# Optimization experiments

Hardware: AMD Instinct MI355X
Metric: run time of the kernel (lower is better)

Reference implementation:

```python
import jax, jax.numpy as jnp
import numpy as np

B, LQ, LK, D, H, DFF = 2, 2048, 2048, 512, 8, 2048


def _xavier(key, shape):
    fan_in, fan_out = shape[0], shape[1]
    lim = float(np.sqrt(6.0 / (fan_in + fan_out)))
    return jax.random.uniform(key, shape, jnp.float32, -lim, lim)


def setup_inputs() -> dict:
    key = jax.random.key(0)
    ks = jax.random.split(key, 8)
    return {
        "inputs": jax.random.normal(ks[0], (B, LQ, D), jnp.float32),
        "encoder_x": jax.random.normal(ks[1], (B, LK, D), jnp.float32),
        "Wq": _xavier(ks[2], (D, D)),
        "Wk": _xavier(ks[3], (D, D)),
        "Wv": _xavier(ks[4], (D, D)),
        "ln1_g": jnp.ones((D,), jnp.float32),
        "ln1_b": jnp.zeros((D,), jnp.float32),
        "W1": jax.random.normal(ks[5], (D, DFF), jnp.float32) * 0.02,
        "b1": jnp.zeros((DFF,), jnp.float32),
        "W2": jax.random.normal(ks[6], (DFF, D), jnp.float32) * 0.02,
        "b2": jnp.zeros((D,), jnp.float32),
        "ln2_g": jnp.ones((D,), jnp.float32),
        "ln2_b": jnp.zeros((D,), jnp.float32),
        "n_heads": H,
    }


def _layer_norm(x, g, b, eps=1e-5):
    mu = jnp.mean(x, axis=-1, keepdims=True)
    var = jnp.var(x, axis=-1, keepdims=True)
    return (x - mu) * jax.lax.rsqrt(var + eps) * g + b


def reference(inputs, encoder_x, Wq, Wk, Wv, ln1_g, ln1_b, W1, b1, W2, b2, ln2_g, ln2_b, n_heads):
    b, lq, d = inputs.shape
    lk = encoder_x.shape[1]
    hd = d // n_heads
    q = (inputs @ Wq).reshape(b, lq, n_heads, hd)
    k = (encoder_x @ Wk).reshape(b, lk, n_heads, hd)
    v = (encoder_x @ Wv).reshape(b, lk, n_heads, hd)
    # scores: [b, h, lq, lk]; scale by sqrt(head_dim) as in source
    scores = jnp.einsum("bqhd,bkhd->bhqk", q, k) / jnp.sqrt(jnp.asarray(hd, q.dtype))
    attn = jax.nn.softmax(scores, axis=-1)
    o = jnp.einsum("bhqk,bkhd->bqhd", attn, v).reshape(b, lq, d)
    out = _layer_norm(o + inputs, ln1_g, ln1_b)
    ff = jax.nn.relu(out @ W1 + b1) @ W2 + b2
    return _layer_norm(ff + out, ln2_g, ln2_b)
```

## Files before the change

kernel.cpp:

```cpp
#include <hip/hip_runtime.h>

typedef __bf16 bf16_t;
typedef __bf16 bf16x8 __attribute__((ext_vector_type(8)));
typedef __bf16 bf16x4 __attribute__((ext_vector_type(4)));
typedef float f32x4 __attribute__((ext_vector_type(4)));
typedef float f32x16 __attribute__((ext_vector_type(16)));
typedef unsigned int u32;

#define GLB_AS(p) ((const __attribute__((address_space(1))) unsigned int*)(p))
#define LDS_AS(p) ((__attribute__((address_space(3))) unsigned int*)(p))

#define SPLIT_ROWS 32768
#define KLD 68
#define VLD 44

__global__ void cvt_both_kernel(const float* __restrict__ inA, bf16_t* __restrict__ outA, float scaleA,
                                const float* __restrict__ inB, bf16_t* __restrict__ outB)
{
    const int bid = blockIdx.x;
    const float* in;
    bf16_t* out;
    float scale;
    int i;
    if (bid < 2048) { in = inA; out = outA; scale = scaleA; i = (bid * 256 + threadIdx.x) * 4; }
    else            { in = inB; out = outB; scale = 1.0f;  i = ((bid - 2048) * 256 + threadIdx.x) * 4; }
    float4 v = *(const float4*)(in + i);
    bf16x4 o;
    o[0] = (bf16_t)(v.x * scale); o[1] = (bf16_t)(v.y * scale);
    o[2] = (bf16_t)(v.z * scale); o[3] = (bf16_t)(v.w * scale);
    *(bf16x4*)(out + i) = o;
}

__global__ void wtrans_all_kernel(const float* __restrict__ Wq, const float* __restrict__ Wk,
                                  const float* __restrict__ Wv, const float* __restrict__ W1,
                                  const float* __restrict__ W2, bf16_t* __restrict__ Wqkvt,
                                  bf16_t* __restrict__ W1t, bf16_t* __restrict__ W2t)
{
    const int j = blockIdx.x;
    const float* in;
    bf16_t* out;
    int R, C, bx, by;
    if (j < 768) {
        int k = j >> 8, l = j & 255;
        in = (k == 0) ? Wq : (k == 1) ? Wk : Wv;
        out = Wqkvt + k * 512 * 512;
        R = 512; C = 512; bx = l & 15; by = l >> 4;
    } else if (j < 1792) {
        int l = j - 768;
        in = W1; out = W1t; R = 512; C = 2048; bx = l % 64; by = l / 64;
    } else {
        int l = j - 1792;
        in = W2; out = W2t; R = 2048; C = 512; bx = l % 16; by = l / 16;
    }
    __shared__ float tile[32][33];
    const int tid = threadIdx.x;
    const int r0 = by * 32, c0 = bx * 32;
#pragma unroll
    for (int t = 0; t < 4; t++) {
        int r = t * 8 + (tid >> 5), c = tid & 31;
        tile[r][c] = in[(size_t)(r0 + r) * C + c0 + c];
    }
    __syncthreads();
#pragma unroll
    for (int t = 0; t < 4; t++) {
        int c = t * 8 + (tid >> 5), r = tid & 31;
        out[(size_t)(c0 + c) * R + r0 + r] = (bf16_t)tile[r][c];
    }
}

__global__ void vtrans_kernel(const bf16_t* __restrict__ qkv, bf16_t* __restrict__ vt)
{
    __shared__ bf16_t t[64][68];
    const int tid = threadIdx.x;
    const int lk0 = blockIdx.x * 64;
    const int bh = blockIdx.y, b = bh >> 3, h = bh & 7;
#pragma unroll
    for (int j = 0; j < 16; j++) {
        int e = j * 256 + tid;
        int lk_i = e >> 6, d = e & 63;
        t[lk_i][d] = qkv[(size_t)(b * 2048 + lk0 + lk_i) * 1536 + 1024 + h * 64 + d];
    }
    __syncthreads();
#pragma unroll
    for (int j = 0; j < 16; j++) {
        int e = j * 256 + tid;
        int d_i = e >> 6, lk = e & 63;
        vt[((size_t)bh * 64 + d_i) * 2048 + lk0 + lk] = t[lk][d_i];
    }
}

template<int BM, bool SPLITA, bool BIAS, bool RELU, bool OUTBF16>
__global__ __launch_bounds__(256)
void gemm_kernel(const bf16_t* __restrict__ A0, const bf16_t* __restrict__ A1, int nsplit,
                 const bf16_t* __restrict__ Bt, const float* __restrict__ bias,
                 void* __restrict__ Cout, int K, int ldC)
{
    constexpr int FR = BM / 32;
    __shared__ __align__(16) bf16_t As[BM * 32];
    __shared__ __align__(16) bf16_t Bs[128 * 32];
    const int bm = blockIdx.x, bn = blockIdx.y;
    const bf16_t* A = (!SPLITA || bn < nsplit) ? A0 : A1;
    const int tid = threadIdx.x;
    const int lane = tid & 63;
    const int wid = tid >> 6;
    const int wr = wid >> 1, wc = wid & 1;

    f32x4 acc[FR][4] = {};

    const int cb = wid * 2;
    const int lbB0 = cb * 1024 + lane * 16;
    const int rowB0 = lbB0 >> 6, colB0 = (lbB0 & 63) >> 1;
    const int rowB1 = (lbB0 + 1024) >> 6, colB1 = ((lbB0 + 1024) & 63) >> 1;
    const int lbA0 = (BM == 128 ? cb * 1024 : wid * 1024) + lane * 16;
    const int rowA0 = lbA0 >> 6, colA0 = (lbA0 & 63) >> 1;
    const int rowA1 = (lbA0 + 1024) >> 6, colA1 = ((lbA0 + 1024) & 63) >> 1;

    const bf16_t* Abase = A + (size_t)(bm * BM) * K;
    const bf16_t* Bbase = Bt + (size_t)(bn * 128) * K;

    for (int k0 = 0; k0 < K; k0 += 32) {
        if constexpr (BM == 128) {
            __builtin_amdgcn_global_load_lds(GLB_AS(Abase + (size_t)rowA0 * K + k0 + colA0), LDS_AS(As + cb * 512), 16, 0, 0);
            __builtin_amdgcn_global_load_lds(GLB_AS(Abase + (size_t)rowA1 * K + k0 + colA1), LDS_AS(As + cb * 512 + 512), 16, 0, 0);
        } else {
            __builtin_amdgcn_global_load_lds(GLB_AS(Abase + (size_t)rowA0 * K + k0 + colA0), LDS_AS(As + wid * 512), 16, 0, 0);
        }
        __builtin_amdgcn_global_load_lds(GLB_AS(Bbase + (size_t)rowB0 * K + k0 + colB0), LDS_AS(Bs + cb * 512), 16, 0, 0);
        __builtin_amdgcn_global_load_lds(GLB_AS(Bbase + (size_t)rowB1 * K + k0 + colB1), LDS_AS(Bs + cb * 512 + 512), 16, 0, 0);
        __syncthreads();
        bf16x8 af[FR], bfr[4];
#pragma unroll
        for (int f = 0; f < FR; f++)
            af[f] = *(const bf16x8*)&As[(wr * (BM / 2) + f * 16 + (lane & 15)) * 32 + (lane >> 4) * 8];
#pragma unroll
        for (int f = 0; f < 4; f++)
            bfr[f] = *(const bf16x8*)&Bs[(wc * 64 + f * 16 + (lane & 15)) * 32 + (lane >> 4) * 8];
#pragma unroll
        for (int fr = 0; fr < FR; fr++)
#pragma unroll
            for (int fc = 0; fc < 4; fc++)
                acc[fr][fc] = __builtin_amdgcn_mfma_f32_16x16x32_bf16(af[fr], bfr[fc], acc[fr][fc], 0, 0, 0);
        __syncthreads();
    }

    const int rg = (lane >> 4) * 4, cl = lane & 15;
#pragma unroll
    for (int fc = 0; fc < 4; fc++) {
        const int col = bn * 128 + wc * 64 + fc * 16 + cl;
        float bv = 0.f;
        if (BIAS) bv = bias[col];
#pragma unroll
        for (int fr = 0; fr < FR; fr++) {
#pragma unroll
            for (int r = 0; r < 4; r++) {
                int rowg = bm * BM + wr * (BM / 2) + fr * 16 + rg + r;
                float v = acc[fr][fc][r] + bv;
                if (RELU) v = fmaxf(v, 0.f);
                if (OUTBF16) ((bf16_t*)Cout)[(size_t)rowg * ldC + col] = (bf16_t)v;
                else         ((float*)Cout)[(size_t)rowg * ldC + col] = v;
            }
        }
    }
}

union BU { bf16x8 v; u32 d[4]; };

static __device__ __forceinline__ u32 pkbf(float a, float b)
{
    union { bf16_t h[2]; u32 w; } u;
    u.h[0] = (bf16_t)a; u.h[1] = (bf16_t)b;
    return u.w;
}

__global__ __launch_bounds__(256)
void flash_kernel(const bf16_t* __restrict__ QKV, const bf16_t* __restrict__ Vt,
                  bf16_t* __restrict__ Op01, bf16_t* __restrict__ Op23,
                  float2* __restrict__ ml)
{
    const int tid = threadIdx.x, lane = tid & 63, wid = tid >> 6;
    const int bh = blockIdx.y, b = bh >> 3, h = bh & 7;
    const int split = blockIdx.z;
    const int qbase = blockIdx.x * 128 + wid * 32;
    const int l31 = lane & 31, hi = lane >> 5;

    __shared__ __align__(16) bf16_t Kst[2][32 * KLD];
    __shared__ __align__(16) bf16_t Vst[2][64 * VLD];
    __shared__ __align__(16) bf16_t tlds[4][32 * 68];
    bf16_t* tw = &tlds[wid][0];

    const bf16_t* Qp = QKV + (size_t)(b * 2048 + qbase + l31) * 1536 + h * 64 + hi * 8;
    const bf16_t* Kbase = QKV + (size_t)(b * 2048) * 1536 + 512 + h * 64;
    const bf16_t* Vbase = Vt + (size_t)bh * 64 * 2048;

    const int kr = tid >> 3, kc = (tid & 7) * 8;
    const int vr = tid >> 2, vc = (tid & 3) * 8;

    bf16x8 qf[4];
#pragma unroll
    for (int t = 0; t < 4; t++)
        qf[t] = *(const bf16x8*)(Qp + t * 16);

    f32x16 acc0 = {}, acc1 = {};
    float mrun = -1e30f, lsum = 0.f;

    const int kv0 = split * 512;

    bf16x8 kreg = *(const bf16x8*)(Kbase + (size_t)(kv0 + kr) * 1536 + kc);
    bf16x8 vreg = *(const bf16x8*)(Vbase + (size_t)vr * 2048 + kv0 + vc);
    *(bf16x8*)&Kst[0][kr * KLD + kc] = kreg;
    *(bf16x8*)&Vst[0][vr * VLD + vc] = vreg;
    __syncthreads();

    int buf = 0;
#pragma unroll 2
    for (int kt = kv0; kt < kv0 + 512; kt += 32) {
        const bool nxt = (kt + 32 < kv0 + 512);
        if (nxt) {
            kreg = *(const bf16x8*)(Kbase + (size_t)(kt + 32 + kr) * 1536 + kc);
            vreg = *(const bf16x8*)(Vbase + (size_t)vr * 2048 + kt + 32 + vc);
        }

        bf16x8 kf[4];
#pragma unroll
        for (int t = 0; t < 4; t++)
            kf[t] = *(const bf16x8*)&Kst[buf][l31 * KLD + hi * 8 + t * 16];
        bf16x8 vf00 = *(const bf16x8*)&Vst[buf][l31 * VLD + hi * 8];
        bf16x8 vf01 = *(const bf16x8*)&Vst[buf][l31 * VLD + 16 + hi * 8];
        bf16x8 vf10 = *(const bf16x8*)&Vst[buf][(32 + l31) * VLD + hi * 8];
        bf16x8 vf11 = *(const bf16x8*)&Vst[buf][(32 + l31) * VLD + 16 + hi * 8];

        f32x16 p = {};
        __builtin_amdgcn_s_setprio(1);
        p = __builtin_amdgcn_mfma_f32_32x32x16_bf16(kf[0], qf[0], p, 0, 0, 0);
        p = __builtin_amdgcn_mfma_f32_32x32x16_bf16(kf[1], qf[1], p, 0, 0, 0);
        p = __builtin_amdgcn_mfma_f32_32x32x16_bf16(kf[2], qf[2], p, 0, 0, 0);
        p = __builtin_amdgcn_mfma_f32_32x32x16_bf16(kf[3], qf[3], p, 0, 0, 0);
        __builtin_amdgcn_s_setprio(0);

        float x0 = fmaxf(p[0], p[8]),  x1 = fmaxf(p[1], p[9]);
        float x2 = fmaxf(p[2], p[10]), x3 = fmaxf(p[3], p[11]);
        float x4 = fmaxf(p[4], p[12]), x5 = fmaxf(p[5], p[13]);
        float x6 = fmaxf(p[6], p[14]), x7 = fmaxf(p[7], p[15]);
        x0 = fmaxf(x0, x4); x1 = fmaxf(x1, x5); x2 = fmaxf(x2, x6); x3 = fmaxf(x3, x7);
        float cm = fmaxf(fmaxf(x0, x1), fmaxf(x2, x3));
        cm = fmaxf(cm, __shfl_xor(cm, 32));

        if (__any(cm > mrun + 12.0f)) {
            float mnew = fmaxf(mrun, cm);
            float fac = __builtin_amdgcn_exp2f(mrun - mnew);
#pragma unroll
            for (int i = 0; i < 16; i++) { acc0[i] *= fac; acc1[i] *= fac; }
            lsum *= fac;
            mrun = mnew;
        }

        float e[16];
#pragma unroll
        for (int i = 0; i < 16; i++) e[i] = __builtin_amdgcn_exp2f(p[i] - mrun);

        float s0 = (e[0] + e[8]) + (e[1] + e[9]);
        float s1 = (e[2] + e[10]) + (e[3] + e[11]);
        float s2 = (e[4] + e[12]) + (e[5] + e[13]);
        float s3 = (e[6] + e[14]) + (e[7] + e[15]);
        float ts = (s0 + s1) + (s2 + s3);
        ts += __shfl_xor(ts, 32);
        lsum += ts;

        u32 pk0 = pkbf(e[0], e[1]),   pk1 = pkbf(e[2], e[3]);
        u32 pk2 = pkbf(e[4], e[5]),   pk3 = pkbf(e[6], e[7]);
        u32 pk4 = pkbf(e[8], e[9]),   pk5 = pkbf(e[10], e[11]);
        u32 pk6 = pkbf(e[12], e[13]), pk7 = pkbf(e[14], e[15]);
        u32 s0w = __shfl_xor(pk0, 32), s1w = __shfl_xor(pk1, 32);
        u32 s2w = __shfl_xor(pk2, 32), s3w = __shfl_xor(pk3, 32);
        u32 s4w = __shfl_xor(pk4, 32), s5w = __shfl_xor(pk5, 32);
        u32 s6w = __shfl_xor(pk6, 32), s7w = __shfl_xor(pk7, 32);

        BU b0, b1;
        b0.d[0] = hi ? s2w : pk0;  b0.d[1] = hi ? s3w : pk1;
        b0.d[2] = hi ? pk2 : s0w;  b0.d[3] = hi ? pk3 : s1w;
        b1.d[0] = hi ? s6w : pk4;  b1.d[1] = hi ? s7w : pk5;
        b1.d[2] = hi ? pk6 : s4w;  b1.d[3] = hi ? pk7 : s5w;

        __builtin_amdgcn_s_setprio(1);
        acc0 = __builtin_amdgcn_mfma_f32_32x32x16_bf16(vf00, b0.v, acc0, 0, 0, 0);
        acc0 = __builtin_amdgcn_mfma_f32_32x32x16_bf16(vf01, b1.v, acc0, 0, 0, 0);
        acc1 = __builtin_amdgcn_mfma_f32_32x32x16_bf16(vf10, b0.v, acc1, 0, 0, 0);
        acc1 = __builtin_amdgcn_mfma_f32_32x32x16_bf16(vf11, b1.v, acc1, 0, 0, 0);
        __builtin_amdgcn_s_setprio(0);

        if (nxt) {
            *(bf16x8*)&Kst[buf ^ 1][kr * KLD + kc] = kreg;
            *(bf16x8*)&Vst[buf ^ 1][vr * VLD + vc] = vreg;
        }
        __syncthreads();
        buf ^= 1;
    }

    float inv = 1.f / lsum;
#pragma unroll
    for (int r = 0; r < 16; r++) {
        int drow = (r & 3) + 8 * (r >> 2) + 4 * hi;
        tw[l31 * 68 + drow]      = (bf16_t)(acc0[r] * inv);
        tw[l31 * 68 + 32 + drow] = (bf16_t)(acc1[r] * inv);
    }
    bf16_t* Op = (split < 2) ? Op01 + (size_t)split * SPLIT_ROWS * 64
                             : Op23 + (size_t)(split - 2) * SPLIT_ROWS * 64;
    const size_t rowbase = (size_t)bh * 2048 + qbase;
#pragma unroll
    for (int ps = 0; ps < 4; ps++) {
        int rr = (lane >> 3) + ps * 8;
        int cc = lane & 7;
        bf16x8 ov = *(const bf16x8*)&tw[rr * 68 + cc * 8];
        *(bf16x8*)(Op + (rowbase + rr) * 64 + cc * 8) = ov;
    }
    if (lane < 32)
        ml[(size_t)split * SPLIT_ROWS + rowbase + l31] = make_float2(mrun, lsum);
}

__global__ __launch_bounds__(256)
void combine_kernel(const bf16_t* __restrict__ Op01, const bf16_t* __restrict__ Op23,
                    const float2* __restrict__ ml, float* __restrict__ O)
{
    int t = blockIdx.x * 256 + threadIdx.x;
    int dim = t & 63;
    int row = t >> 6;
    int bh = row >> 11, qrow = row & 2047;
    float2 m0 = ml[row];
    float2 m1 = ml[SPLIT_ROWS + row];
    float2 m2 = ml[2 * SPLIT_ROWS + row];
    float2 m3 = ml[3 * SPLIT_ROWS + row];
    float M = fmaxf(fmaxf(m0.x, m1.x), fmaxf(m2.x, m3.x));
    float w0 = m0.y * __builtin_amdgcn_exp2f(m0.x - M);
    float w1 = m1.y * __builtin_amdgcn_exp2f(m1.x - M);
    float w2 = m2.y * __builtin_amdgcn_exp2f(m2.x - M);
    float w3 = m3.y * __builtin_amdgcn_exp2f(m3.x - M);
    float o = (w0 * (float)Op01[(size_t)row * 64 + dim]
             + w1 * (float)Op01[(size_t)(SPLIT_ROWS + row) * 64 + dim]
             + w2 * (float)Op23[(size_t)row * 64 + dim]
             + w3 * (float)Op23[(size_t)(SPLIT_ROWS + row) * 64 + dim]) / (w0 + w1 + w2 + w3);
    int b = bh >> 3, h = bh & 7;
    O[((size_t)(b * 2048 + qrow)) * 512 + h * 64 + dim] = o;
}

template<bool RESBF>
__global__ __launch_bounds__(128)
void add_ln_kernel(const float* __restrict__ a, const void* __restrict__ res,
                   const float* __restrict__ g, const float* __restrict__ bta,
                   float* outf, bf16_t* outb)
{
    const int row = blockIdx.x, tid = threadIdx.x;
    const float4* a4 = (const float4*)(a + (size_t)row * 512);
    float4 av = a4[tid];
    float r0, r1, r2, r3;
    if (RESBF) {
        bf16x4 rv = ((const bf16x4*)res)[row * 128 + tid];
        r0 = (float)rv[0]; r1 = (float)rv[1]; r2 = (float)rv[2]; r3 = (float)rv[3];
    } else {
        float4 rv = ((const float4*)res)[row * 128 + tid];
        r0 = rv.x; r1 = rv.y; r2 = rv.z; r3 = rv.w;
    }
    float x0 = av.x + r0, x1 = av.y + r1, x2 = av.z + r2, x3 = av.w + r3;
    float s = x0 + x1 + x2 + x3;
    float sq = x0 * x0 + x1 * x1 + x2 * x2 + x3 * x3;
#pragma unroll
    for (int d = 1; d < 64; d <<= 1) { s += __shfl_xor(s, d); sq += __shfl_xor(sq, d); }
    __shared__ float red[2][2];
    const int wid = tid >> 6;
    if ((tid & 63) == 0) { red[wid][0] = s; red[wid][1] = sq; }
    __syncthreads();
    s = red[0][0] + red[1][0];
    sq = red[0][1] + red[1][1];
    float mu = s * (1.f / 512.f);
    float var = sq * (1.f / 512.f) - mu * mu;
    float rstd = rsqrtf(var + 1e-5f);
    const float4* g4 = (const float4*)g;
    const float4* b4 = (const float4*)bta;
    float4 gv = g4[tid], bv = b4[tid];
    float4 y;
    y.x = (x0 - mu) * rstd * gv.x + bv.x;
    y.y = (x1 - mu) * rstd * gv.y + bv.y;
    y.z = (x2 - mu) * rstd * gv.z + bv.z;
    y.w = (x3 - mu) * rstd * gv.w + bv.w;
    if (outf) ((float4*)(outf + (size_t)row * 512))[tid] = y;
    if (outb) {
        bf16x4 o;
        o[0] = (bf16_t)y.x; o[1] = (bf16_t)y.y; o[2] = (bf16_t)y.z; o[3] = (bf16_t)y.w;
        *(bf16x4*)(outb + (size_t)row * 512 + tid * 4) = o;
    }
}

extern "C" void kernel_launch(void* const* d_in, const int* in_sizes, int n_in,
                              void* d_out, int out_size, void* d_ws, size_t ws_size,
                              hipStream_t stream)
{
    const float* inputs = (const float*)d_in[0];
    const float* encx   = (const float*)d_in[1];
    const float* Wq     = (const float*)d_in[2];
    const float* Wk     = (const float*)d_in[3];
    const float* Wv     = (const float*)d_in[4];
    const float* ln1g   = (const float*)d_in[5];
    const float* ln1b   = (const float*)d_in[6];
    const float* W1     = (const float*)d_in[7];
    const float* b1     = (const float*)d_in[8];
    const float* W2     = (const float*)d_in[9];
    const float* b2     = (const float*)d_in[10];
    const float* ln2g   = (const float*)d_in[11];
    const float* ln2b   = (const float*)d_in[12];

    char* ws = (char*)d_ws;
    const size_t MB = 1u << 20;
    bf16_t* W1t   = (bf16_t*)(ws);
    bf16_t* W2t   = (bf16_t*)(ws + 2 * MB);
    bf16_t* Xb    = (bf16_t*)(ws + 4 * MB);
    bf16_t* Op01  = (bf16_t*)(ws + 4 * MB);
    bf16_t* out1b = (bf16_t*)(ws + 4 * MB);
    bf16_t* Eb    = (bf16_t*)(ws + 8 * MB);
    bf16_t* QKVb  = (bf16_t*)(ws + 12 * MB);
    float*  Obuf  = (float*)(ws + 12 * MB);
    bf16_t* Hb    = (bf16_t*)(ws + 12 * MB);
    bf16_t* Vtb   = (bf16_t*)(ws + 24 * MB);
    bf16_t* Wqkvt = (bf16_t*)(ws + 28 * MB);
    float2* mlbuf = (float2*)(ws + 28 * MB);
    bf16_t* Op23  = (bf16_t*)d_out;
    float*  FF    = (float*)d_out;

    cvt_both_kernel<<<4096, 256, 0, stream>>>(inputs, Xb, 0.125f * 1.44269504f, encx, Eb);
    wtrans_all_kernel<<<2816, 256, 0, stream>>>(Wq, Wk, Wv, W1, W2, Wqkvt, W1t, W2t);
    gemm_kernel<64, true, false, false, true><<<dim3(64, 12), 256, 0, stream>>>(
        Xb, Eb, 4, Wqkvt, nullptr, QKVb, 512, 1536);
    vtrans_kernel<<<dim3(32, 16), 256, 0, stream>>>(QKVb, Vtb);
    flash_kernel<<<dim3(16, 16, 4), 256, 0, stream>>>(QKVb, Vtb, Op01, Op23, mlbuf);
    combine_kernel<<<8192, 256, 0, stream>>>(Op01, Op23, mlbuf, Obuf);
    add_ln_kernel<false><<<4096, 128, 0, stream>>>(Obuf, inputs, ln1g, ln1b, nullptr, out1b);
    gemm_kernel<128, false, true, true, true><<<dim3(32, 16), 256, 0, stream>>>(
        out1b, nullptr, 0, W1t, b1, Hb, 512, 2048);
    gemm_kernel<64, false, true, false, false><<<dim3(64, 4), 256, 0, stream>>>(
        Hb, nullptr, 0, W2t, b2, FF, 2048, 512);
    add_ln_kernel<true><<<4096, 128, 0, stream>>>(FF, out1b, ln2g, ln2b, (float*)d_out, nullptr);
}
```

Before: 141.3 us.

## Fuse split-combine with LayerNorm and move softmax row sums onto MFMA

Merges the flash-decoding split combine with the first residual-add LayerNorm into one kernel, so the fp32 attention output buffer is never written to or read back from global memory. Inside the flash kernel, the cross-half shuffles are replaced with permlane32_swap when that builtin exists. The softmax denominator is now accumulated by extra MFMAs against a ones vector instead of VALU adds and a shuffle. This adds two MFMAs and 16 accumulator registers per iteration, and the row sum is now computed from bf16-rounded probabilities. The workspace buffers are remapped to fit the new layout.

```diff
diff --git a/kernel.cpp b/kernel.cpp
--- a/kernel.cpp
+++ b/kernel.cpp
@@ -6,6 +6,7 @@
 typedef float f32x4 __attribute__((ext_vector_type(4)));
 typedef float f32x16 __attribute__((ext_vector_type(16)));
 typedef unsigned int u32;
+typedef unsigned int u32x2 __attribute__((ext_vector_type(2)));
 
 #define GLB_AS(p) ((const __attribute__((address_space(1))) unsigned int*)(p))
 #define LDS_AS(p) ((__attribute__((address_space(3))) unsigned int*)(p))
@@ -172,6 +173,19 @@
     return u.w;
 }
 
+static __device__ __forceinline__ void plswap(u32 a, u32 b, u32& x, u32& y)
+{
+#if __has_builtin(__builtin_amdgcn_permlane32_swap)
+    u32x2 r = __builtin_amdgcn_permlane32_swap(a, b, false, false);
+    x = r[0]; y = r[1];
+#else
+    const bool hi = (threadIdx.x & 32) != 0;
+    u32 sb = __shfl_xor(b, 32), sa = __shfl_xor(a, 32);
+    x = hi ? sb : a;
+    y = hi ? b : sa;
+#endif
+}
+
 __global__ __launch_bounds__(256)
 void flash_kernel(const bf16_t* __restrict__ QKV, const bf16_t* __restrict__ Vt,
                   bf16_t* __restrict__ Op01, bf16_t* __restrict__ Op23,
@@ -200,8 +214,12 @@
     for (int t = 0; t < 4; t++)
         qf[t] = *(const bf16x8*)(Qp + t * 16);
 
-    f32x16 acc0 = {}, acc1 = {};
-    float mrun = -1e30f, lsum = 0.f;
+    bf16x8 ones;
+#pragma unroll
+    for (int e = 0; e < 8; e++) ones[e] = (bf16_t)1.0f;
+
+    f32x16 acc0 = {}, acc1 = {}, accS = {};
+    float mrun = -1e30f;
 
     const int kv0 = split * 512;
 
@@ -243,49 +261,41 @@
         float x6 = fmaxf(p[6], p[14]), x7 = fmaxf(p[7], p[15]);
         x0 = fmaxf(x0, x4); x1 = fmaxf(x1, x5); x2 = fmaxf(x2, x6); x3 = fmaxf(x3, x7);
         float cm = fmaxf(fmaxf(x0, x1), fmaxf(x2, x3));
-        cm = fmaxf(cm, __shfl_xor(cm, 32));
+        {
+            u32 r0, r1;
+            plswap(__float_as_uint(cm), __float_as_uint(cm), r0, r1);
+            cm = fmaxf(__uint_as_float(r0), __uint_as_float(r1));
+        }
 
         if (__any(cm > mrun + 12.0f)) {
             float mnew = fmaxf(mrun, cm);
             float fac = __builtin_amdgcn_exp2f(mrun - mnew);
 #pragma unroll
-            for (int i = 0; i < 16; i++) { acc0[i] *= fac; acc1[i] *= fac; }
-            lsum *= fac;
+            for (int i = 0; i < 16; i++) { acc0[i] *= fac; acc1[i] *= fac; accS[i] *= fac; }
             mrun = mnew;
         }
 
         float e[16];
 #pragma unroll
         for (int i = 0; i < 16; i++) e[i] = __builtin_amdgcn_exp2f(p[i] - mrun);
-
-        float s0 = (e[0] + e[8]) + (e[1] + e[9]);
-        float s1 = (e[2] + e[10]) + (e[3] + e[11]);
-        float s2 = (e[4] + e[12]) + (e[5] + e[13]);
-        float s3 = (e[6] + e[14]) + (e[7] + e[15]);
-        float ts = (s0 + s1) + (s2 + s3);
-        ts += __shfl_xor(ts, 32);
-        lsum += ts;
 
         u32 pk0 = pkbf(e[0], e[1]),   pk1 = pkbf(e[2], e[3]);
         u32 pk2 = pkbf(e[4], e[5]),   pk3 = pkbf(e[6], e[7]);
         u32 pk4 = pkbf(e[8], e[9]),   pk5 = pkbf(e[10], e[11]);
         u32 pk6 = pkbf(e[12], e[13]), pk7 = pkbf(e[14], e[15]);
-        u32 s0w = __shfl_xor(pk0, 32), s1w = __shfl_xor(pk1, 32);
-        u32 s2w = __shfl_xor(pk2, 32), s3w = __shfl_xor(pk3, 32);
-        u32 s4w = __shfl_xor(pk4, 32), s5w = __shfl_xor(pk5, 32);
-        u32 s6w = __shfl_xor(pk6, 32), s7w = __shfl_xor(pk7, 32);
-
         BU b0, b1;
-        b0.d[0] = hi ? s2w : pk0;  b0.d[1] = hi ? s3w : pk1;
-        b0.d[2] = hi ? pk2 : s0w;  b0.d[3] = hi ? pk3 : s1w;
-        b1.d[0] = hi ? s6w : pk4;  b1.d[1] = hi ? s7w : pk5;
-        b1.d[2] = hi ? pk6 : s4w;  b1.d[3] = hi ? pk7 : s5w;
+        plswap(pk0, pk2, b0.d[0], b0.d[2]);
+        plswap(pk1, pk3, b0.d[1], b0.d[3]);
+        plswap(pk4, pk6, b1.d[0], b1.d[2]);
+        plswap(pk5, pk7, b1.d[1], b1.d[3]);
 
         __builtin_amdgcn_s_setprio(1);
         acc0 = __builtin_amdgcn_mfma_f32_32x32x16_bf16(vf00, b0.v, acc0, 0, 0, 0);
         acc0 = __builtin_amdgcn_mfma_f32_32x32x16_bf16(vf01, b1.v, acc0, 0, 0, 0);
         acc1 = __builtin_amdgcn_mfma_f32_32x32x16_bf16(vf10, b0.v, acc1, 0, 0, 0);
         acc1 = __builtin_amdgcn_mfma_f32_32x32x16_bf16(vf11, b1.v, acc1, 0, 0, 0);
+        accS = __builtin_amdgcn_mfma_f32_32x32x16_bf16(ones, b0.v, accS, 0, 0, 0);
+        accS = __builtin_amdgcn_mfma_f32_32x32x16_bf16(ones, b1.v, accS, 0, 0, 0);
         __builtin_amdgcn_s_setprio(0);
 
         if (nxt) {
@@ -296,6 +306,7 @@
         buf ^= 1;
     }
 
+    const float lsum = accS[0];
     float inv = 1.f / lsum;
 #pragma unroll
     for (int r = 0; r < 16; r++) {
@@ -317,29 +328,61 @@
         ml[(size_t)split * SPLIT_ROWS + rowbase + l31] = make_float2(mrun, lsum);
 }
 
-__global__ __launch_bounds__(256)
-void combine_kernel(const bf16_t* __restrict__ Op01, const bf16_t* __restrict__ Op23,
-                    const float2* __restrict__ ml, float* __restrict__ O)
-{
-    int t = blockIdx.x * 256 + threadIdx.x;
-    int dim = t & 63;
-    int row = t >> 6;
-    int bh = row >> 11, qrow = row & 2047;
-    float2 m0 = ml[row];
-    float2 m1 = ml[SPLIT_ROWS + row];
-    float2 m2 = ml[2 * SPLIT_ROWS + row];
-    float2 m3 = ml[3 * SPLIT_ROWS + row];
+__global__ __launch_bounds__(128)
+void combine_ln_kernel(const bf16_t* __restrict__ Op01, const bf16_t* __restrict__ Op23,
+                       const float2* __restrict__ ml, const float* __restrict__ resid,
+                       const float* __restrict__ g, const float* __restrict__ bta,
+                       bf16_t* __restrict__ outb)
+{
+    const int row = blockIdx.x;
+    const int tid = threadIdx.x;
+    const int b = row >> 11, q = row & 2047;
+    const int d = tid * 4, h = d >> 6, dd = d & 63;
+    const size_t prow = ((size_t)(b * 8 + h)) * 2048 + q;
+
+    float2 m0 = ml[prow];
+    float2 m1 = ml[SPLIT_ROWS + prow];
+    float2 m2 = ml[2 * SPLIT_ROWS + prow];
+    float2 m3 = ml[3 * SPLIT_ROWS + prow];
     float M = fmaxf(fmaxf(m0.x, m1.x), fmaxf(m2.x, m3.x));
     float w0 = m0.y * __builtin_amdgcn_exp2f(m0.x - M);
     float w1 = m1.y * __builtin_amdgcn_exp2f(m1.x - M);
     float w2 = m2.y * __builtin_amdgcn_exp2f(m2.x - M);
     float w3 = m3.y * __builtin_amdgcn_exp2f(m3.x - M);
-    float o = (w0 * (float)Op01[(size_t)row * 64 + dim]
-             + w1 * (float)Op01[(size_t)(SPLIT_ROWS + row) * 64 + dim]
-             + w2 * (float)Op23[(size_t)row * 64 + dim]
-             + w3 * (float)Op23[(size_t)(SPLIT_ROWS + row) * 64 + dim]) / (w0 + w1 + w2 + w3);
-    int b = bh >> 3, h = bh & 7;
-    O[((size_t)(b * 2048 + qrow)) * 512 + h * 64 + dim] = o;
+    float winv = 1.f / (w0 + w1 + w2 + w3);
+
+    bf16x4 p0 = *(const bf16x4*)(Op01 + prow * 64 + dd);
+    bf16x4 p1 = *(const bf16x4*)(Op01 + (SPLIT_ROWS + prow) * 64 + dd);
+    bf16x4 p2 = *(const bf16x4*)(Op23 + prow * 64 + dd);
+    bf16x4 p3 = *(const bf16x4*)(Op23 + (SPLIT_ROWS + prow) * 64 + dd);
+    float4 rv = ((const float4*)resid)[row * 128 + tid];
+
+    float x0 = (w0 * (float)p0[0] + w1 * (float)p1[0] + w2 * (float)p2[0] + w3 * (float)p3[0]) * winv + rv.x;
+    float x1 = (w0 * (float)p0[1] + w1 * (float)p1[1] + w2 * (float)p2[1] + w3 * (float)p3[1]) * winv + rv.y;
+    float x2 = (w0 * (float)p0[2] + w1 * (float)p1[2] + w2 * (float)p2[2] + w3 * (float)p3[2]) * winv + rv.z;
+    float x3 = (w0 * (float)p0[3] + w1 * (float)p1[3] + w2 * (float)p2[3] + w3 * (float)p3[3]) * winv + rv.w;
+
+    float s = x0 + x1 + x2 + x3;
+    float sq = x0 * x0 + x1 * x1 + x2 * x2 + x3 * x3;
+#pragma unroll
+    for (int dl = 1; dl < 64; dl <<= 1) { s += __shfl_xor(s, dl); sq += __shfl_xor(sq, dl); }
+    __shared__ float red[2][2];
+    const int wid = tid >> 6;
+    if ((tid & 63) == 0) { red[wid][0] = s; red[wid][1] = sq; }
+    __syncthreads();
+    s = red[0][0] + red[1][0];
+    sq = red[0][1] + red[1][1];
+    float mu = s * (1.f / 512.f);
+    float var = sq * (1.f / 512.f) - mu * mu;
+    float rstd = rsqrtf(var + 1e-5f);
+    const float4 gv = ((const float4*)g)[tid];
+    const float4 bv = ((const float4*)bta)[tid];
+    bf16x4 o;
+    o[0] = (bf16_t)((x0 - mu) * rstd * gv.x + bv.x);
+    o[1] = (bf16_t)((x1 - mu) * rstd * gv.y + bv.y);
+    o[2] = (bf16_t)((x2 - mu) * rstd * gv.z + bv.z);
+    o[3] = (bf16_t)((x3 - mu) * rstd * gv.w + bv.w);
+    *(bf16x4*)(outb + (size_t)row * 512 + tid * 4) = o;
 }
 
 template<bool RESBF>
@@ -413,12 +456,11 @@
     bf16_t* W2t   = (bf16_t*)(ws + 2 * MB);
     bf16_t* Xb    = (bf16_t*)(ws + 4 * MB);
     bf16_t* Op01  = (bf16_t*)(ws + 4 * MB);
-    bf16_t* out1b = (bf16_t*)(ws + 4 * MB);
+    bf16_t* Hb    = (bf16_t*)(ws + 4 * MB);
     bf16_t* Eb    = (bf16_t*)(ws + 8 * MB);
     bf16_t* QKVb  = (bf16_t*)(ws + 12 * MB);
-    float*  Obuf  = (float*)(ws + 12 * MB);
-    bf16_t* Hb    = (bf16_t*)(ws + 12 * MB);
     bf16_t* Vtb   = (bf16_t*)(ws + 24 * MB);
+    bf16_t* out1b = (bf16_t*)(ws + 24 * MB);
     bf16_t* Wqkvt = (bf16_t*)(ws + 28 * MB);
     float2* mlbuf = (float2*)(ws + 28 * MB);
     bf16_t* Op23  = (bf16_t*)d_out;
@@ -430,8 +472,7 @@
         Xb, Eb, 4, Wqkvt, nullptr, QKVb, 512, 1536);
     vtrans_kernel<<<dim3(32, 16), 256, 0, stream>>>(QKVb, Vtb);
     flash_kernel<<<dim3(16, 16, 4), 256, 0, stream>>>(QKVb, Vtb, Op01, Op23, mlbuf);
-    combine_kernel<<<8192, 256, 0, stream>>>(Op01, Op23, mlbuf, Obuf);
-    add_ln_kernel<false><<<4096, 128, 0, stream>>>(Obuf, inputs, ln1g, ln1b, nullptr, out1b);
+    combine_ln_kernel<<<4096, 128, 0, stream>>>(Op01, Op23, mlbuf, inputs, ln1g, ln1b, out1b);
     gemm_kernel<128, false, true, true, true><<<dim3(32, 16), 256, 0, stream>>>(
         out1b, nullptr, 0, W1t, b1, Hb, 512, 2048);
     gemm_kernel<64, false, true, false, false><<<dim3(64, 4), 256, 0, stream>>>(
```

New measurement: 135.0 us. 4.5% less time.
